# Kernel tuning notes

Hardware: AMD Instinct MI355X
Metric: run time of the kernel (lower is better)

Reference implementation:

```python
import jax, jax.numpy as jnp
import numpy as np

NHEAD = 16      # config['transformer_nheads']
N_LAYERS = 2    # config['layers']
EPS = 1e-5      # torch LayerNorm default


def _layernorm(x, w, b):
    m = jnp.mean(x, axis=-1, keepdims=True)
    v = jnp.var(x, axis=-1, keepdims=True)
    return (x - m) * jax.lax.rsqrt(v + EPS) * w + b


def _mha_causal(h, wqkv, bqkv, wo, bo):
    # Causal self-attention == running the encoder on every growing prefix and
    # keeping the last position (the original O(T^2) python loop), since the
    # encoder layer has no positional encoding and all other ops are per-token.
    B, T, H = h.shape
    hd = H // NHEAD
    qkv = h @ wqkv.T + bqkv                       # [B,T,3H]
    q, k, v = jnp.split(qkv, 3, axis=-1)
    q = q.reshape(B, T, NHEAD, hd)
    k = k.reshape(B, T, NHEAD, hd)
    v = v.reshape(B, T, NHEAD, hd)
    scale = jnp.asarray(1.0 / np.sqrt(hd), h.dtype)
    scores = jnp.einsum('bqhd,bkhd->bhqk', q, k) * scale
    mask = jnp.tril(jnp.ones((T, T), dtype=bool))  # query q attends to keys <= q
    scores = jnp.where(mask, scores, jnp.asarray(-1e9, h.dtype))
    attn = jax.nn.softmax(scores, axis=-1)
    out = jnp.einsum('bhqk,bkhd->bqhd', attn, v).reshape(B, T, H)
    return out @ wo.T + bo


def _encoder_layer(h, in_proj_w, in_proj_b, out_proj_w, out_proj_b,
                   ln1_w, ln1_b, ff1_w, ff1_b, ff2_w, ff2_b, ln2_w, ln2_b):
    # PyTorch TransformerEncoderLayer, post-norm, relu, eval mode (no dropout)
    a = _mha_causal(h, in_proj_w, in_proj_b, out_proj_w, out_proj_b)
    h = _layernorm(h + a, ln1_w, ln1_b)
    f = jax.nn.relu(h @ ff1_w.T + ff1_b) @ ff2_w.T + ff2_b
    return _layernorm(h + f, ln2_w, ln2_b)


def _lstm(xs, h0, c0, w_ih, w_hh, b_ih, b_hh):
    # PyTorch single-layer LSTM, gate order (i, f, g, o)
    def step(carry, x_t):
        h, c = carry
        g = x_t @ w_ih.T + b_ih + h @ w_hh.T + b_hh
        i, f, gg, o = jnp.split(g, 4, axis=-1)
        c = jax.nn.sigmoid(f) * c + jax.nn.sigmoid(i) * jnp.tanh(gg)
        h = jax.nn.sigmoid(o) * jnp.tanh(c)
        return (h, c), h
    (hT, cT), ys = jax.lax.scan(step, (h0, c0), jnp.swapaxes(xs, 0, 1))
    return jnp.swapaxes(ys, 0, 1), hT, cT


def _forward(x, user_vector, game_vector, fc_w, fc_b,
             in_proj_w, in_proj_b, out_proj_w, out_proj_b,
             ln1_w, ln1_b, ff1_w, ff1_b, ff2_w, ff2_b, ln2_w, ln2_b,
             lstm_w_ih, lstm_w_hh, lstm_b_ih, lstm_b_hh,
             out1_w, out1_b, out2_w, out2_b):
    h = jax.nn.relu(x @ fc_w.T + fc_b)            # fc (dropout off in eval)
    uv, gv = user_vector, game_vector
    lstm_out = h
    for j in range(N_LAYERS):
        enc = _encoder_layer(h, in_proj_w, in_proj_b, out_proj_w, out_proj_b,
                             ln1_w, ln1_b, ff1_w, ff1_b, ff2_w, ff2_b, ln2_w, ln2_b)
        lstm_out, hT, cT = _lstm(enc, uv[:, j, :], gv[:, j, :],
                                 lstm_w_ih, lstm_w_hh, lstm_b_ih, lstm_b_hh)
        h = lstm_out
        uv = uv.at[:, j, :].set(hT)
        gv = gv.at[:, j, :].set(cT)
    o = jax.nn.relu(lstm_out @ out1_w.T + out1_b) @ out2_w.T + out2_b
    return jax.nn.log_softmax(o, axis=-1), gv, uv


def setup_inputs() -> dict:
    B, T, D, H, FF, OUT = 256, 10, 512, 1024, 2048, 2
    L = N_LAYERS
    key = jax.random.key(0)
    ks = jax.random.split(key, 20)
    def w(k, shape, fan_in):
        return (jax.random.normal(k, shape, jnp.float32) / np.sqrt(fan_in)).astype(jnp.float32)
    z = lambda shape: jnp.zeros(shape, jnp.float32)
    return {
        'x': jax.random.normal(ks[0], (B, T, D), jnp.float32),
        'user_vector': jax.random.normal(ks[1], (B, L, H), jnp.float32),
        'game_vector': jax.random.normal(ks[2], (B, L, H), jnp.float32),
        'fc_w': w(ks[3], (H, D), D), 'fc_b': z((H,)),
        'in_proj_w': w(ks[4], (3 * H, H), H), 'in_proj_b': z((3 * H,)),
        'out_proj_w': w(ks[5], (H, H), H), 'out_proj_b': z((H,)),
        'ln1_w': jnp.ones((H,), jnp.float32), 'ln1_b': z((H,)),
        'ff1_w': w(ks[6], (FF, H), H), 'ff1_b': z((FF,)),
        'ff2_w': w(ks[7], (H, FF), FF), 'ff2_b': z((H,)),
        'ln2_w': jnp.ones((H,), jnp.float32), 'ln2_b': z((H,)),
        'lstm_w_ih': w(ks[8], (4 * H, H), H), 'lstm_w_hh': w(ks[9], (4 * H, H), H),
        'lstm_b_ih': z((4 * H,)), 'lstm_b_hh': z((4 * H,)),
        'out1_w': w(ks[10], (H // 2, H), H), 'out1_b': z((H // 2,)),
        'out2_w': w(ks[11], (OUT, H // 2), H // 2), 'out2_b': z((OUT,)),
    }


def reference(x, user_vector, game_vector, fc_w, fc_b,
              in_proj_w, in_proj_b, out_proj_w, out_proj_b,
              ln1_w, ln1_b, ff1_w, ff1_b, ff2_w, ff2_b, ln2_w, ln2_b,
              lstm_w_ih, lstm_w_hh, lstm_b_ih, lstm_b_hh,
              out1_w, out1_b, out2_w, out2_b):
    return _forward(x, user_vector, game_vector, fc_w, fc_b,
                    in_proj_w, in_proj_b, out_proj_w, out_proj_b,
                    ln1_w, ln1_b, ff1_w, ff1_b, ff2_w, ff2_b, ln2_w, ln2_b,
                    lstm_w_ih, lstm_w_hh, lstm_b_ih, lstm_b_hh,
                    out1_w, out1_b, out2_w, out2_b)
```

## Files before the change

### kernel.cpp

```cpp
#include <hip/hip_runtime.h>
#include <math.h>

#define B_    256
#define T_    10
#define D_    512
#define H_    1024
#define FF_   2048
#define NHEAD 16
#define HD    64
#define M_    (B_ * T_)
#define NL    2

typedef unsigned short u16;
typedef unsigned int   u32;
typedef __attribute__((ext_vector_type(8))) short bf16x8;
typedef __attribute__((ext_vector_type(4))) float f32x4;

__device__ inline float sigmoidf_(float x) { return 1.0f / (1.0f + expf(-x)); }
__device__ inline float b2f(u16 v) { return __uint_as_float(((u32)v) << 16); }
__device__ inline u16 f2b(float f) {
    u32 u = __float_as_uint(f);
    return (u16)((u + 0x7fffu + ((u >> 16) & 1u)) >> 16);
}

struct u16x8 { u16 v[8]; };

__global__ __launch_bounds__(256) void cvt_weights(
    const float* __restrict__ fcw, const float* __restrict__ inp,
    const float* __restrict__ outp, const float* __restrict__ f1,
    const float* __restrict__ f2, const float* __restrict__ wih,
    const float* __restrict__ whh, const float* __restrict__ o1w,
    const float* __restrict__ xin,
    u16* __restrict__ wb)
{
    const int e = (blockIdx.x * 256 + threadIdx.x) * 8;
    const float* src; int off;
    if      (e <   524288) { src = fcw;  off = 0; }
    else if (e <  3670016) { src = inp;  off = 524288; }
    else if (e <  4718592) { src = outp; off = 3670016; }
    else if (e <  6815744) { src = f1;   off = 4718592; }
    else if (e <  8912896) { src = f2;   off = 6815744; }
    else if (e < 13107200) { src = wih;  off = 8912896; }
    else if (e < 17301504) { src = whh;  off = 13107200; }
    else if (e < 17825792) { src = o1w;  off = 17301504; }
    else                   { src = xin;  off = 17825792; }
    const float* p = src + (e - off);
    const float4 x0 = *((const float4*)p);
    const float4 x1 = *((const float4*)(p + 4));
    u16x8 r;
    r.v[0] = f2b(x0.x); r.v[1] = f2b(x0.y); r.v[2] = f2b(x0.z); r.v[3] = f2b(x0.w);
    r.v[4] = f2b(x1.x); r.v[5] = f2b(x1.y); r.v[6] = f2b(x1.z); r.v[7] = f2b(x1.w);
    *((u16x8*)(wb + e)) = r;
}

template<int BM, int BN, bool RELU, bool WF32, bool WB16>
__global__ __launch_bounds__(256) void gemm_mfma(const u16* __restrict__ A,
                                                 const u16* __restrict__ W,
                                                 const float* __restrict__ bias,
                                                 float* __restrict__ Cf,
                                                 u16* __restrict__ Cb,
                                                 int M, int N, int K)
{
    constexpr int MI = BM / 32;
    constexpr int NJ = BN / 32;
    constexpr int ASZ = 2 * BM * 32;
    constexpr int BSZ = 2 * BN * 32;
    __shared__ alignas(16) u16 As[2 * ASZ];
    __shared__ alignas(16) u16 Bs[2 * BSZ];

    int bx, by;
    {
        const int gx = gridDim.x, gy = gridDim.y;
        const int total = gx * gy;
        const int id = blockIdx.y * gx + blockIdx.x;
        if (((total & 7) == 0) && ((gy & 3) == 0)) {
            const int per = total >> 3;
            const int lid = (id & 7) * per + (id >> 3);
            const int band = gx << 2;
            const int g = lid / band;
            const int r = lid - g * band;
            by = (g << 2) + (r & 3);
            bx = r >> 2;
        } else { bx = blockIdx.x; by = blockIdx.y; }
    }

    const int wave = threadIdx.x >> 6;
    const int lane = threadIdx.x & 63;
    const int m0 = by * BM;
    const int n0 = bx * BN;
    const int wm = (wave >> 1) * (BM / 2);
    const int wn = (wave & 1) * (BN / 2);
    const int lr = lane >> 2;
    const int lc = (lane & 3) * 8;
    const int fr = lane & 15;
    const int kq = lane >> 4;

    auto stage = [&](int buf, int k0) {
#pragma unroll
        for (int cc = 0; cc < BM / 64; ++cc) {
            const int c = cc * 4 + wave;
            const u16* g = A + (size_t)(m0 + c * 16 + lr) * K + k0 + lc;
#pragma unroll
            for (int kk = 0; kk < 2; ++kk)
                __builtin_amdgcn_global_load_lds(
                    (const __attribute__((address_space(1))) void*)(g + kk * 32),
                    (__attribute__((address_space(3))) void*)(As + buf * ASZ + kk * BM * 32 + c * 512), 16, 0, 0);
        }
#pragma unroll
        for (int cc = 0; cc < BN / 64; ++cc) {
            const int c = cc * 4 + wave;
            const u16* g = W + (size_t)(n0 + c * 16 + lr) * K + k0 + lc;
#pragma unroll
            for (int kk = 0; kk < 2; ++kk)
                __builtin_amdgcn_global_load_lds(
                    (const __attribute__((address_space(1))) void*)(g + kk * 32),
                    (__attribute__((address_space(3))) void*)(Bs + buf * BSZ + kk * BN * 32 + c * 512), 16, 0, 0);
        }
    };

    f32x4 acc[MI][NJ] = {};

    stage(0, 0);
    __syncthreads();
    int cur = 0;
    for (int k0 = 0; k0 < K; k0 += 64) {
        if (k0 + 64 < K) stage(cur ^ 1, k0 + 64);
#pragma unroll
        for (int kk = 0; kk < 2; ++kk) {
            bf16x8 a[MI], b[NJ];
#pragma unroll
            for (int i = 0; i < MI; ++i)
                a[i] = *(const bf16x8*)(As + cur * ASZ + kk * BM * 32 + (wm + i * 16 + fr) * 32 + kq * 8);
#pragma unroll
            for (int j = 0; j < NJ; ++j)
                b[j] = *(const bf16x8*)(Bs + cur * BSZ + kk * BN * 32 + (wn + j * 16 + fr) * 32 + kq * 8);
#pragma unroll
            for (int i = 0; i < MI; ++i)
#pragma unroll
                for (int j = 0; j < NJ; ++j)
                    acc[i][j] = __builtin_amdgcn_mfma_f32_16x16x32_bf16(a[i], b[j], acc[i][j], 0, 0, 0);
        }
        __syncthreads();
        cur ^= 1;
    }

#pragma unroll
    for (int i = 0; i < MI; ++i) {
#pragma unroll
        for (int j = 0; j < NJ; ++j) {
            const int col = n0 + wn + j * 16 + fr;
            const float bv = bias ? bias[col] : 0.0f;
#pragma unroll
            for (int r = 0; r < 4; ++r) {
                const int row = m0 + wm + i * 16 + kq * 4 + r;
                float v = acc[i][j][r] + bv;
                if (RELU) v = fmaxf(v, 0.0f);
                if (WF32) Cf[(size_t)row * N + col] = v;
                if (WB16) Cb[(size_t)row * N + col] = f2b(v);
            }
        }
    }
}

__global__ __launch_bounds__(256) void lstm_step(const u16* __restrict__ h_in,
                                                 const u16* __restrict__ Whh,
                                                 const u16* __restrict__ gx,
                                                 const float* __restrict__ bih,
                                                 const float* __restrict__ bhh,
                                                 float* __restrict__ cstate,
                                                 u16* __restrict__ h_out,
                                                 float* __restrict__ lout_f,
                                                 u16* __restrict__ lout_b,
                                                 int t,
                                                 float* __restrict__ hT_out,
                                                 float* __restrict__ cT_out)
{
    __shared__ alignas(16) u16 smem[2 * 16384];
    float* ghs = (float*)smem;

    const int j0 = blockIdx.x * 16;
    const int b0 = blockIdx.y * 64;

    const int wave = threadIdx.x >> 6;
    const int lane = threadIdx.x & 63;
    const int wm = (wave >> 1) * 32;
    const int wn = (wave & 1) * 32;
    const int lr = lane >> 2;
    const int lc = (lane & 3) * 8;
    const int fr = lane & 15;
    const int kq = lane >> 4;

    auto stage = [&](int buf, int k0) {
        const u16* ga = h_in + (size_t)(b0 + wave * 16 + lr) * H_ + k0 + lc;
#pragma unroll
        for (int kk = 0; kk < 4; ++kk)
            __builtin_amdgcn_global_load_lds(
                (const __attribute__((address_space(1))) void*)(ga + kk * 32),
                (__attribute__((address_space(3))) void*)(smem + buf * 16384 + kk * 2048 + wave * 512), 16, 0, 0);
        const u16* gb = Whh + (size_t)(wave * H_ + j0 + lr) * H_ + k0 + lc;
#pragma unroll
        for (int kk = 0; kk < 4; ++kk)
            __builtin_amdgcn_global_load_lds(
                (const __attribute__((address_space(1))) void*)(gb + kk * 32),
                (__attribute__((address_space(3))) void*)(smem + buf * 16384 + 8192 + kk * 2048 + wave * 512), 16, 0, 0);
    };

    f32x4 acc[2][2] = {};

    stage(0, 0);
    __syncthreads();
    int cur = 0;
    for (int k0 = 0; k0 < H_; k0 += 128) {
        if (k0 + 128 < H_) stage(cur ^ 1, k0 + 128);
        const u16* As = smem + cur * 16384;
        const u16* Bs = As + 8192;
#pragma unroll
        for (int kk = 0; kk < 4; ++kk) {
            bf16x8 a[2], b[2];
#pragma unroll
            for (int i = 0; i < 2; ++i)
                a[i] = *(const bf16x8*)(As + kk * 2048 + (wm + i * 16 + fr) * 32 + kq * 8);
#pragma unroll
            for (int j = 0; j < 2; ++j)
                b[j] = *(const bf16x8*)(Bs + kk * 2048 + (wn + j * 16 + fr) * 32 + kq * 8);
#pragma unroll
            for (int i = 0; i < 2; ++i)
#pragma unroll
                for (int j = 0; j < 2; ++j)
                    acc[i][j] = __builtin_amdgcn_mfma_f32_16x16x32_bf16(a[i], b[j], acc[i][j], 0, 0, 0);
        }
        __syncthreads();
        cur ^= 1;
    }

#pragma unroll
    for (int i = 0; i < 2; ++i)
#pragma unroll
        for (int j = 0; j < 2; ++j) {
            const int rl = wn + j * 16 + fr;
#pragma unroll
            for (int r = 0; r < 4; ++r) {
                const int bl = wm + i * 16 + kq * 4 + r;
                ghs[bl * 65 + rl] = acc[i][j][r];
            }
        }
    __syncthreads();

    {
        const int bl = threadIdx.x >> 2;
        const int jq = threadIdx.x & 3;
        const int b_ = b0 + bl;
        const int jbase = jq * 4;
        const u16* g1 = gx + (size_t)(b_ * T_ + t) * (4 * H_) + j0 + jbase;
        float hh4[4], c4[4];
#pragma unroll
        for (int q = 0; q < 4; ++q) {
            const int jj = jbase + q;
            const int jg = j0 + jbase + q;
            const float gi = b2f(g1[q])          + bih[jg]           + bhh[jg]           + ghs[bl * 65 +  0 + jj];
            const float gf = b2f(g1[H_ + q])     + bih[H_ + jg]      + bhh[H_ + jg]      + ghs[bl * 65 + 16 + jj];
            const float gg = b2f(g1[2 * H_ + q]) + bih[2 * H_ + jg]  + bhh[2 * H_ + jg]  + ghs[bl * 65 + 32 + jj];
            const float go = b2f(g1[3 * H_ + q]) + bih[3 * H_ + jg]  + bhh[3 * H_ + jg]  + ghs[bl * 65 + 48 + jj];
            const int sid = b_ * H_ + jg;
            const float c  = sigmoidf_(gf) * cstate[sid] + sigmoidf_(gi) * tanhf(gg);
            const float hh = sigmoidf_(go) * tanhf(c);
            cstate[sid] = c;
            c4[q] = c;
            hh4[q] = hh;
        }
        u16*   hp = h_out  + (size_t)b_ * H_ + j0 + jbase;
        float* lf = lout_f + (size_t)(b_ * T_ + t) * H_ + j0 + jbase;
        u16*   lb = lout_b + (size_t)(b_ * T_ + t) * H_ + j0 + jbase;
#pragma unroll
        for (int q = 0; q < 4; ++q) {
            const u16 hb16 = f2b(hh4[q]);
            hp[q] = hb16;
            lf[q] = hh4[q];
            lb[q] = hb16;
        }
        if (hT_out) {
#pragma unroll
            for (int q = 0; q < 4; ++q) {
                hT_out[(size_t)b_ * (NL * H_) + j0 + jbase + q] = hh4[q];
                cT_out[(size_t)b_ * (NL * H_) + j0 + jbase + q] = c4[q];
            }
        }
    }
}

__global__ __launch_bounds__(256) void attn_kernel(const u16* __restrict__ qkv,
                                                   u16* __restrict__ ctx)
{
    const int bh = blockIdx.x;
    const int b  = bh >> 4;
    const int h  = bh & 15;

    __shared__ float q[T_][HD], k[T_][HD], v[T_][HD];
    __shared__ float p[T_][T_];

    for (int idx = threadIdx.x; idx < T_ * HD; idx += 256) {
        const int t = idx >> 6, d = idx & 63;
        const u16* row = qkv + (size_t)(b * T_ + t) * (3 * H_) + h * HD + d;
        q[t][d] = b2f(row[0]);
        k[t][d] = b2f(row[H_]);
        v[t][d] = b2f(row[2 * H_]);
    }
    __syncthreads();

    if (threadIdx.x < T_ * T_) {
        const int qi = threadIdx.x / T_, ki = threadIdx.x % T_;
        float s = 0.0f;
        if (ki <= qi) {
            for (int d = 0; d < HD; ++d) s = fmaf(q[qi][d], k[ki][d], s);
            s *= 0.125f;
        }
        p[qi][ki] = s;
    }
    __syncthreads();

    if (threadIdx.x < T_) {
        const int rq = threadIdx.x;
        float mx = -1e30f;
        for (int ki = 0; ki <= rq; ++ki) mx = fmaxf(mx, p[rq][ki]);
        float sum = 0.0f;
        for (int ki = 0; ki <= rq; ++ki) { const float e = expf(p[rq][ki] - mx); p[rq][ki] = e; sum += e; }
        const float inv = 1.0f / sum;
        for (int ki = 0; ki <= rq; ++ki) p[rq][ki] *= inv;
        for (int ki = rq + 1; ki < T_; ++ki) p[rq][ki] = 0.0f;
    }
    __syncthreads();

    for (int idx = threadIdx.x; idx < T_ * HD; idx += 256) {
        const int t = idx >> 6, d = idx & 63;
        float s = 0.0f;
        for (int ki = 0; ki <= t; ++ki) s = fmaf(p[t][ki], v[ki][d], s);
        ctx[(size_t)(b * T_ + t) * H_ + h * HD + d] = f2b(s);
    }
}

__global__ __launch_bounds__(256) void ln_kernel(const float* __restrict__ x,
                                                 const float* __restrict__ res,
                                                 const float* __restrict__ w,
                                                 const float* __restrict__ b,
                                                 float* __restrict__ outf,
                                                 u16* __restrict__ outb)
{
    const int row = blockIdx.x;
    const float* xr = x + (size_t)row * H_;
    const float* rr = res + (size_t)row * H_;

    float vals[4];
    float s = 0.0f, s2 = 0.0f;
#pragma unroll
    for (int i = 0; i < 4; ++i) {
        const int c = threadIdx.x + i * 256;
        const float vv = xr[c] + rr[c];
        vals[i] = vv;
        s += vv;
        s2 = fmaf(vv, vv, s2);
    }
    for (int off = 32; off; off >>= 1) {
        s  += __shfl_down(s, off);
        s2 += __shfl_down(s2, off);
    }
    __shared__ float rs_[4], rs2_[4];
    const int wave = threadIdx.x >> 6, lane = threadIdx.x & 63;
    if (lane == 0) { rs_[wave] = s; rs2_[wave] = s2; }
    __syncthreads();
    const float st  = rs_[0] + rs_[1] + rs_[2] + rs_[3];
    const float st2 = rs2_[0] + rs2_[1] + rs2_[2] + rs2_[3];
    const float m   = st * (1.0f / 1024.0f);
    const float var = st2 * (1.0f / 1024.0f) - m * m;
    const float rsv = rsqrtf(var + 1e-5f);
#pragma unroll
    for (int i = 0; i < 4; ++i) {
        const int c = threadIdx.x + i * 256;
        const float v = (vals[i] - m) * rsv * w[c] + b[c];
        if (outf) outf[(size_t)row * H_ + c] = v;
        if (outb) outb[(size_t)row * H_ + c] = f2b(v);
    }
}

__global__ __launch_bounds__(256) void init_states(const float* __restrict__ uvec,
                                                   const float* __restrict__ gvec,
                                                   int layer,
                                                   u16* __restrict__ hstate_b,
                                                   float* __restrict__ cstate)
{
    const int id = blockIdx.x * 256 + threadIdx.x;
    const int b  = id >> 10;
    const int j  = id & 1023;
    hstate_b[id] = f2b(uvec[(size_t)(b * NL + layer) * H_ + j]);
    cstate[id]   = gvec[(size_t)(b * NL + layer) * H_ + j];
}

__global__ __launch_bounds__(256) void head_kernel(const float* __restrict__ o1,
                                                   const float* __restrict__ w2,
                                                   const float* __restrict__ b2,
                                                   float* __restrict__ out)
{
    const int token = blockIdx.x * 4 + (threadIdx.x >> 6);
    const int lane  = threadIdx.x & 63;
    const float* row = o1 + (size_t)token * (H_ / 2);
    float s0 = 0.0f, s1 = 0.0f;
    for (int c = lane; c < H_ / 2; c += 64) {
        const float xv = row[c];
        s0 = fmaf(xv, w2[c], s0);
        s1 = fmaf(xv, w2[H_ / 2 + c], s1);
    }
    for (int off = 32; off; off >>= 1) {
        s0 += __shfl_down(s0, off);
        s1 += __shfl_down(s1, off);
    }
    if (lane == 0) {
        const float o0 = s0 + b2[0];
        const float o1v = s1 + b2[1];
        const float mx = fmaxf(o0, o1v);
        const float lse = mx + logf(expf(o0 - mx) + expf(o1v - mx));
        out[(size_t)token * 2 + 0] = o0 - lse;
        out[(size_t)token * 2 + 1] = o1v - lse;
    }
}

extern "C" void kernel_launch(void* const* d_in, const int* in_sizes, int n_in,
                              void* d_out, int out_size, void* d_ws, size_t ws_size,
                              hipStream_t stream)
{
    const float* x         = (const float*)d_in[0];
    const float* user_vec  = (const float*)d_in[1];
    const float* game_vec  = (const float*)d_in[2];
    const float* fc_w      = (const float*)d_in[3];
    const float* fc_b      = (const float*)d_in[4];
    const float* in_proj_w = (const float*)d_in[5];
    const float* in_proj_b = (const float*)d_in[6];
    const float* out_proj_w= (const float*)d_in[7];
    const float* out_proj_b= (const float*)d_in[8];
    const float* ln1_w     = (const float*)d_in[9];
    const float* ln1_b     = (const float*)d_in[10];
    const float* ff1_w     = (const float*)d_in[11];
    const float* ff1_b     = (const float*)d_in[12];
    const float* ff2_w     = (const float*)d_in[13];
    const float* ff2_b     = (const float*)d_in[14];
    const float* ln2_w     = (const float*)d_in[15];
    const float* ln2_b     = (const float*)d_in[16];
    const float* w_ih      = (const float*)d_in[17];
    const float* w_hh      = (const float*)d_in[18];
    const float* b_ih      = (const float*)d_in[19];
    const float* b_hh      = (const float*)d_in[20];
    const float* out1_w    = (const float*)d_in[21];
    const float* out1_b    = (const float*)d_in[22];
    const float* out2_w    = (const float*)d_in[23];
    const float* out2_b    = (const float*)d_in[24];
    float* out = (float*)d_out;

    char* base = (char*)d_ws;
    u16* wb = (u16*)base;
    u16* fc_wb   = wb;
    u16* inp_wb  = wb + 524288;
    u16* outp_wb = wb + 3670016;
    u16* ff1_wb  = wb + 4718592;
    u16* ff2_wb  = wb + 6815744;
    u16* wih_b   = wb + 8912896;
    u16* whh_b   = wb + 13107200;
    u16* out1_wb = wb + 17301504;
    u16* x_b     = wb + 17825792;
    char* A1 = base + 38273024;
    char* S1 = A1 + 20971520;
    char* S2 = S1 + 10485760;
    u16*  hb = (u16*)(S2 + 5242880);
    float* buf0 = (float*)((char*)hb + 5242880);
    float* cstate = (float*)((char*)buf0 + 10485760);
    u16*  hs0 = (u16*)((char*)cstate + 1048576);
    u16*  hs1 = (u16*)((char*)hs0 + 524288);

    u16*   qkv_b = (u16*)A1;
    float* tmp1  = (float*)A1;
    float* tmp2  = (float*)(A1 + 10485760);
    u16*   gx_b  = (u16*)A1;
    float* o1    = (float*)A1;
    u16*   ff1b  = (u16*)S1;
    u16*   ctx_b = (u16*)S2;
    u16*   ln1b  = (u16*)S2;
    u16*   enc_b = (u16*)S2;

    float* gv_out = out + (size_t)M_ * 2;
    float* uv_out = gv_out + (size_t)B_ * NL * H_;

    hipLaunchKernelGGL(cvt_weights, dim3(19136512 / 8 / 256), dim3(256), 0, stream,
                       fc_w, in_proj_w, out_proj_w, ff1_w, ff2_w, w_ih, w_hh, out1_w,
                       x, wb);

    hipLaunchKernelGGL((gemm_mfma<64, 128, true, true, true>),
                       dim3(H_ / 128, M_ / 64), dim3(256), 0, stream,
                       x_b, fc_wb, fc_b, buf0, hb, M_, H_, D_);

    for (int layer = 0; layer < NL; ++layer) {
        hipLaunchKernelGGL((gemm_mfma<128, 128, false, false, true>),
                           dim3(3 * H_ / 128, M_ / 128), dim3(256), 0, stream,
                           hb, inp_wb, in_proj_b, (float*)nullptr, qkv_b, M_, 3 * H_, H_);
        hipLaunchKernelGGL(attn_kernel, dim3(B_ * NHEAD), dim3(256), 0, stream, qkv_b, ctx_b);
        hipLaunchKernelGGL((gemm_mfma<64, 128, false, true, false>),
                           dim3(H_ / 128, M_ / 64), dim3(256), 0, stream,
                           ctx_b, outp_wb, out_proj_b, tmp1, (u16*)nullptr, M_, H_, H_);
        hipLaunchKernelGGL(ln_kernel, dim3(M_), dim3(256), 0, stream,
                           buf0, tmp1, ln1_w, ln1_b, tmp2, ln1b);
        hipLaunchKernelGGL((gemm_mfma<128, 128, true, false, true>),
                           dim3(FF_ / 128, M_ / 128), dim3(256), 0, stream,
                           ln1b, ff1_wb, ff1_b, (float*)nullptr, ff1b, M_, FF_, H_);
        hipLaunchKernelGGL((gemm_mfma<64, 128, false, true, false>),
                           dim3(H_ / 128, M_ / 64), dim3(256), 0, stream,
                           ff1b, ff2_wb, ff2_b, tmp1, (u16*)nullptr, M_, H_, FF_);
        hipLaunchKernelGGL(ln_kernel, dim3(M_), dim3(256), 0, stream,
                           tmp2, tmp1, ln2_w, ln2_b, (float*)nullptr, enc_b);
        hipLaunchKernelGGL((gemm_mfma<128, 128, false, false, true>),
                           dim3(4 * H_ / 128, M_ / 128), dim3(256), 0, stream,
                           enc_b, wih_b, (const float*)nullptr, (float*)nullptr, gx_b, M_, 4 * H_, H_);
        hipLaunchKernelGGL(init_states, dim3(B_ * H_ / 256), dim3(256), 0, stream,
                           user_vec, game_vec, layer, hs0, cstate);
        for (int t = 0; t < T_; ++t) {
            const bool last = (t == T_ - 1);
            hipLaunchKernelGGL(lstm_step, dim3(64, 4), dim3(256), 0, stream,
                               (t & 1) ? hs1 : hs0, whh_b, gx_b, b_ih, b_hh, cstate,
                               (t & 1) ? hs0 : hs1, buf0, hb, t,
                               last ? (uv_out + layer * H_) : nullptr,
                               last ? (gv_out + layer * H_) : nullptr);
        }
    }

    hipLaunchKernelGGL((gemm_mfma<64, 64, true, true, false>),
                       dim3((H_ / 2) / 64, M_ / 64), dim3(256), 0, stream,
                       hb, out1_wb, out1_b, o1, (u16*)nullptr, M_, H_ / 2, H_);
    hipLaunchKernelGGL(head_kernel, dim3(M_ / 4), dim3(256), 0, stream, o1, out2_w, out2_b, out);
}
```

Before: 777.8 us.

## Halve GEMM K-tile, split LSTM step finer, vectorize layernorm

The GEMM kernel now stages 32-wide K slices instead of 64, which halves shared memory per block, and it declares launch bounds of 4 blocks per CU to raise occupancy. The LSTM step kernel now covers 8 hidden units per block instead of 16 and launches twice as many blocks, so the small recurrent GEMM spreads across more CUs. The layernorm kernel switches to float4 loads and stores. The trade-off is more K-loop iterations and barriers per GEMM tile, and a possible register cap that could cause spills.

```diff
diff --git a/kernel.cpp b/kernel.cpp
--- a/kernel.cpp
+++ b/kernel.cpp
@@ -24,6 +24,7 @@
 }
 
 struct u16x8 { u16 v[8]; };
+struct u16x4 { u16 v[4]; };
 
 __global__ __launch_bounds__(256) void cvt_weights(
     const float* __restrict__ fcw, const float* __restrict__ inp,
@@ -54,17 +55,17 @@
 }
 
 template<int BM, int BN, bool RELU, bool WF32, bool WB16>
-__global__ __launch_bounds__(256) void gemm_mfma(const u16* __restrict__ A,
-                                                 const u16* __restrict__ W,
-                                                 const float* __restrict__ bias,
-                                                 float* __restrict__ Cf,
-                                                 u16* __restrict__ Cb,
-                                                 int M, int N, int K)
+__global__ __launch_bounds__(256, 4) void gemm_mfma(const u16* __restrict__ A,
+                                                    const u16* __restrict__ W,
+                                                    const float* __restrict__ bias,
+                                                    float* __restrict__ Cf,
+                                                    u16* __restrict__ Cb,
+                                                    int M, int N, int K)
 {
     constexpr int MI = BM / 32;
     constexpr int NJ = BN / 32;
-    constexpr int ASZ = 2 * BM * 32;
-    constexpr int BSZ = 2 * BN * 32;
+    constexpr int ASZ = BM * 32;
+    constexpr int BSZ = BN * 32;
     __shared__ alignas(16) u16 As[2 * ASZ];
     __shared__ alignas(16) u16 Bs[2 * BSZ];
 
@@ -100,21 +101,17 @@
         for (int cc = 0; cc < BM / 64; ++cc) {
             const int c = cc * 4 + wave;
             const u16* g = A + (size_t)(m0 + c * 16 + lr) * K + k0 + lc;
-#pragma unroll
-            for (int kk = 0; kk < 2; ++kk)
-                __builtin_amdgcn_global_load_lds(
-                    (const __attribute__((address_space(1))) void*)(g + kk * 32),
-                    (__attribute__((address_space(3))) void*)(As + buf * ASZ + kk * BM * 32 + c * 512), 16, 0, 0);
+            __builtin_amdgcn_global_load_lds(
+                (const __attribute__((address_space(1))) void*)g,
+                (__attribute__((address_space(3))) void*)(As + buf * ASZ + c * 512), 16, 0, 0);
         }
 #pragma unroll
         for (int cc = 0; cc < BN / 64; ++cc) {
             const int c = cc * 4 + wave;
             const u16* g = W + (size_t)(n0 + c * 16 + lr) * K + k0 + lc;
-#pragma unroll
-            for (int kk = 0; kk < 2; ++kk)
-                __builtin_amdgcn_global_load_lds(
-                    (const __attribute__((address_space(1))) void*)(g + kk * 32),
-                    (__attribute__((address_space(3))) void*)(Bs + buf * BSZ + kk * BN * 32 + c * 512), 16, 0, 0);
+            __builtin_amdgcn_global_load_lds(
+                (const __attribute__((address_space(1))) void*)g,
+                (__attribute__((address_space(3))) void*)(Bs + buf * BSZ + c * 512), 16, 0, 0);
         }
     };
 
@@ -123,23 +120,20 @@
     stage(0, 0);
     __syncthreads();
     int cur = 0;
-    for (int k0 = 0; k0 < K; k0 += 64) {
-        if (k0 + 64 < K) stage(cur ^ 1, k0 + 64);
-#pragma unroll
-        for (int kk = 0; kk < 2; ++kk) {
-            bf16x8 a[MI], b[NJ];
-#pragma unroll
-            for (int i = 0; i < MI; ++i)
-                a[i] = *(const bf16x8*)(As + cur * ASZ + kk * BM * 32 + (wm + i * 16 + fr) * 32 + kq * 8);
+    for (int k0 = 0; k0 < K; k0 += 32) {
+        if (k0 + 32 < K) stage(cur ^ 1, k0 + 32);
+        bf16x8 a[MI], b[NJ];
+#pragma unroll
+        for (int i = 0; i < MI; ++i)
+            a[i] = *(const bf16x8*)(As + cur * ASZ + (wm + i * 16 + fr) * 32 + kq * 8);
+#pragma unroll
+        for (int j = 0; j < NJ; ++j)
+            b[j] = *(const bf16x8*)(Bs + cur * BSZ + (wn + j * 16 + fr) * 32 + kq * 8);
+#pragma unroll
+        for (int i = 0; i < MI; ++i)
 #pragma unroll
             for (int j = 0; j < NJ; ++j)
-                b[j] = *(const bf16x8*)(Bs + cur * BSZ + kk * BN * 32 + (wn + j * 16 + fr) * 32 + kq * 8);
-#pragma unroll
-            for (int i = 0; i < MI; ++i)
-#pragma unroll
-                for (int j = 0; j < NJ; ++j)
-                    acc[i][j] = __builtin_amdgcn_mfma_f32_16x16x32_bf16(a[i], b[j], acc[i][j], 0, 0, 0);
-        }
+                acc[i][j] = __builtin_amdgcn_mfma_f32_16x16x32_bf16(a[i], b[j], acc[i][j], 0, 0, 0);
         __syncthreads();
         cur ^= 1;
     }
@@ -175,16 +169,16 @@
                                                  float* __restrict__ hT_out,
                                                  float* __restrict__ cT_out)
 {
-    __shared__ alignas(16) u16 smem[2 * 16384];
+    __shared__ alignas(16) u16 smem[2 * 12288];
     float* ghs = (float*)smem;
 
-    const int j0 = blockIdx.x * 16;
+    const int j0 = blockIdx.x * 8;
     const int b0 = blockIdx.y * 64;
 
     const int wave = threadIdx.x >> 6;
     const int lane = threadIdx.x & 63;
     const int wm = (wave >> 1) * 32;
-    const int wn = (wave & 1) * 32;
+    const int wn = (wave & 1) * 16;
     const int lr = lane >> 2;
     const int lc = (lane & 3) * 8;
     const int fr = lane & 15;
@@ -196,93 +190,77 @@
         for (int kk = 0; kk < 4; ++kk)
             __builtin_amdgcn_global_load_lds(
                 (const __attribute__((address_space(1))) void*)(ga + kk * 32),
-                (__attribute__((address_space(3))) void*)(smem + buf * 16384 + kk * 2048 + wave * 512), 16, 0, 0);
-        const u16* gb = Whh + (size_t)(wave * H_ + j0 + lr) * H_ + k0 + lc;
-#pragma unroll
-        for (int kk = 0; kk < 4; ++kk)
+                (__attribute__((address_space(3))) void*)(smem + buf * 12288 + kk * 2048 + wave * 512), 16, 0, 0);
+#pragma unroll
+        for (int s = 0; s < 2; ++s) {
+            const int rl = s * 16 + lr;
+            const int grow = (rl >> 3) * H_ + j0 + (rl & 7);
+            const u16* gb = Whh + (size_t)grow * H_ + k0 + wave * 32 + lc;
             __builtin_amdgcn_global_load_lds(
-                (const __attribute__((address_space(1))) void*)(gb + kk * 32),
-                (__attribute__((address_space(3))) void*)(smem + buf * 16384 + 8192 + kk * 2048 + wave * 512), 16, 0, 0);
+                (const __attribute__((address_space(1))) void*)gb,
+                (__attribute__((address_space(3))) void*)(smem + buf * 12288 + 8192 + wave * 1024 + s * 512), 16, 0, 0);
+        }
     };
 
-    f32x4 acc[2][2] = {};
+    f32x4 acc[2] = {};
 
     stage(0, 0);
     __syncthreads();
     int cur = 0;
     for (int k0 = 0; k0 < H_; k0 += 128) {
         if (k0 + 128 < H_) stage(cur ^ 1, k0 + 128);
-        const u16* As = smem + cur * 16384;
+        const u16* As = smem + cur * 12288;
         const u16* Bs = As + 8192;
 #pragma unroll
         for (int kk = 0; kk < 4; ++kk) {
-            bf16x8 a[2], b[2];
+            bf16x8 a[2], b;
 #pragma unroll
             for (int i = 0; i < 2; ++i)
                 a[i] = *(const bf16x8*)(As + kk * 2048 + (wm + i * 16 + fr) * 32 + kq * 8);
-#pragma unroll
-            for (int j = 0; j < 2; ++j)
-                b[j] = *(const bf16x8*)(Bs + kk * 2048 + (wn + j * 16 + fr) * 32 + kq * 8);
+            b = *(const bf16x8*)(Bs + kk * 1024 + (wn + fr) * 32 + kq * 8);
 #pragma unroll
             for (int i = 0; i < 2; ++i)
-#pragma unroll
-                for (int j = 0; j < 2; ++j)
-                    acc[i][j] = __builtin_amdgcn_mfma_f32_16x16x32_bf16(a[i], b[j], acc[i][j], 0, 0, 0);
+                acc[i] = __builtin_amdgcn_mfma_f32_16x16x32_bf16(a[i], b, acc[i], 0, 0, 0);
         }
         __syncthreads();
         cur ^= 1;
     }
 
 #pragma unroll
-    for (int i = 0; i < 2; ++i)
-#pragma unroll
-        for (int j = 0; j < 2; ++j) {
-            const int rl = wn + j * 16 + fr;
-#pragma unroll
-            for (int r = 0; r < 4; ++r) {
-                const int bl = wm + i * 16 + kq * 4 + r;
-                ghs[bl * 65 + rl] = acc[i][j][r];
-            }
-        }
+    for (int i = 0; i < 2; ++i) {
+        const int rl = wn + fr;
+#pragma unroll
+        for (int r = 0; r < 4; ++r) {
+            const int bl = wm + i * 16 + kq * 4 + r;
+            ghs[bl * 33 + rl] = acc[i][r];
+        }
+    }
     __syncthreads();
 
     {
         const int bl = threadIdx.x >> 2;
-        const int jq = threadIdx.x & 3;
+        const int jpair = (threadIdx.x & 3) * 2;
         const int b_ = b0 + bl;
-        const int jbase = jq * 4;
-        const u16* g1 = gx + (size_t)(b_ * T_ + t) * (4 * H_) + j0 + jbase;
-        float hh4[4], c4[4];
-#pragma unroll
-        for (int q = 0; q < 4; ++q) {
-            const int jj = jbase + q;
-            const int jg = j0 + jbase + q;
-            const float gi = b2f(g1[q])          + bih[jg]           + bhh[jg]           + ghs[bl * 65 +  0 + jj];
-            const float gf = b2f(g1[H_ + q])     + bih[H_ + jg]      + bhh[H_ + jg]      + ghs[bl * 65 + 16 + jj];
-            const float gg = b2f(g1[2 * H_ + q]) + bih[2 * H_ + jg]  + bhh[2 * H_ + jg]  + ghs[bl * 65 + 32 + jj];
-            const float go = b2f(g1[3 * H_ + q]) + bih[3 * H_ + jg]  + bhh[3 * H_ + jg]  + ghs[bl * 65 + 48 + jj];
+#pragma unroll
+        for (int q = 0; q < 2; ++q) {
+            const int jj = jpair + q;
+            const int jg = j0 + jj;
+            const u16* g1 = gx + (size_t)(b_ * T_ + t) * (4 * H_) + jg;
+            const float gi = b2f(g1[0])      + bih[jg]          + bhh[jg]          + ghs[bl * 33 +  0 + jj];
+            const float gf = b2f(g1[H_])     + bih[H_ + jg]     + bhh[H_ + jg]     + ghs[bl * 33 +  8 + jj];
+            const float gg = b2f(g1[2 * H_]) + bih[2 * H_ + jg] + bhh[2 * H_ + jg] + ghs[bl * 33 + 16 + jj];
+            const float go = b2f(g1[3 * H_]) + bih[3 * H_ + jg] + bhh[3 * H_ + jg] + ghs[bl * 33 + 24 + jj];
             const int sid = b_ * H_ + jg;
             const float c  = sigmoidf_(gf) * cstate[sid] + sigmoidf_(gi) * tanhf(gg);
             const float hh = sigmoidf_(go) * tanhf(c);
             cstate[sid] = c;
-            c4[q] = c;
-            hh4[q] = hh;
-        }
-        u16*   hp = h_out  + (size_t)b_ * H_ + j0 + jbase;
-        float* lf = lout_f + (size_t)(b_ * T_ + t) * H_ + j0 + jbase;
-        u16*   lb = lout_b + (size_t)(b_ * T_ + t) * H_ + j0 + jbase;
-#pragma unroll
-        for (int q = 0; q < 4; ++q) {
-            const u16 hb16 = f2b(hh4[q]);
-            hp[q] = hb16;
-            lf[q] = hh4[q];
-            lb[q] = hb16;
-        }
-        if (hT_out) {
-#pragma unroll
-            for (int q = 0; q < 4; ++q) {
-                hT_out[(size_t)b_ * (NL * H_) + j0 + jbase + q] = hh4[q];
-                cT_out[(size_t)b_ * (NL * H_) + j0 + jbase + q] = c4[q];
+            const u16 hb16 = f2b(hh);
+            h_out[sid] = hb16;
+            lout_f[(size_t)(b_ * T_ + t) * H_ + jg] = hh;
+            lout_b[(size_t)(b_ * T_ + t) * H_ + jg] = hb16;
+            if (hT_out) {
+                hT_out[(size_t)b_ * (NL * H_) + jg] = hh;
+                cT_out[(size_t)b_ * (NL * H_) + jg] = c;
             }
         }
     }
@@ -346,19 +324,13 @@
                                                  u16* __restrict__ outb)
 {
     const int row = blockIdx.x;
-    const float* xr = x + (size_t)row * H_;
-    const float* rr = res + (size_t)row * H_;
-
-    float vals[4];
+    const int c = threadIdx.x * 4;
+    const float4 xv = *(const float4*)(x + (size_t)row * H_ + c);
+    const float4 rv = *(const float4*)(res + (size_t)row * H_ + c);
+    float vals[4] = { xv.x + rv.x, xv.y + rv.y, xv.z + rv.z, xv.w + rv.w };
     float s = 0.0f, s2 = 0.0f;
 #pragma unroll
-    for (int i = 0; i < 4; ++i) {
-        const int c = threadIdx.x + i * 256;
-        const float vv = xr[c] + rr[c];
-        vals[i] = vv;
-        s += vv;
-        s2 = fmaf(vv, vv, s2);
-    }
+    for (int i = 0; i < 4; ++i) { s += vals[i]; s2 = fmaf(vals[i], vals[i], s2); }
     for (int off = 32; off; off >>= 1) {
         s  += __shfl_down(s, off);
         s2 += __shfl_down(s2, off);
@@ -372,12 +344,17 @@
     const float m   = st * (1.0f / 1024.0f);
     const float var = st2 * (1.0f / 1024.0f) - m * m;
     const float rsv = rsqrtf(var + 1e-5f);
-#pragma unroll
-    for (int i = 0; i < 4; ++i) {
-        const int c = threadIdx.x + i * 256;
-        const float v = (vals[i] - m) * rsv * w[c] + b[c];
-        if (outf) outf[(size_t)row * H_ + c] = v;
-        if (outb) outb[(size_t)row * H_ + c] = f2b(v);
+    const float4 wv = *(const float4*)(w + c);
+    const float4 bv = *(const float4*)(b + c);
+    float o[4];
+    o[0] = (vals[0] - m) * rsv * wv.x + bv.x;
+    o[1] = (vals[1] - m) * rsv * wv.y + bv.y;
+    o[2] = (vals[2] - m) * rsv * wv.z + bv.z;
+    o[3] = (vals[3] - m) * rsv * wv.w + bv.w;
+    if (outf) *(float4*)(outf + (size_t)row * H_ + c) = make_float4(o[0], o[1], o[2], o[3]);
+    if (outb) {
+        u16x4 ob = { { f2b(o[0]), f2b(o[1]), f2b(o[2]), f2b(o[3]) } };
+        *(u16x4*)(outb + (size_t)row * H_ + c) = ob;
     }
 }
 
@@ -519,7 +496,7 @@
                            user_vec, game_vec, layer, hs0, cstate);
         for (int t = 0; t < T_; ++t) {
             const bool last = (t == T_ - 1);
-            hipLaunchKernelGGL(lstm_step, dim3(64, 4), dim3(256), 0, stream,
+            hipLaunchKernelGGL(lstm_step, dim3(128, 4), dim3(256), 0, stream,
                                (t & 1) ? hs1 : hs0, whh_b, gx_b, b_ih, b_hh, cstate,
                                (t & 1) ? hs0 : hs1, buf0, hb, t,
                                last ? (uv_out + layer * H_) : nullptr,
```

After: 831.0 us. 1.07x slower.
